# Optimization experiments

Measured on AMD Instinct MI355X. Metric: run time of the kernel, lower is better.

The kernel has to match this reference:

```python
import jax, jax.numpy as jnp
import numpy as np

DIM = 256          # model dim
HK = 8             # kv heads
HQ = 32            # query heads
H = HQ // HK       # queries per kv group
DH = 128           # head dim (== DIM//2, required by RoPE assert)
B = 1
T = 2048
THETA = 10000.0
CACHE = 8192       # RoPE cached seq_len; module uses _freqs_cis[-T:]


def _rope(x):
    # x: [..., T, DH]; positions are the LAST T of the cached 8192 (faithful to _freqs_cis[-T:])
    t = x.shape[-2]
    half = DH  # == DIM // 2
    pos = jnp.arange(CACHE - t, CACHE, dtype=jnp.float32)
    inv_freq = THETA ** (-(jnp.arange(half, dtype=jnp.float32) / half))
    f = pos[:, None] * inv_freq[None, :]            # [T, DH]
    cos, sin = jnp.cos(f), jnp.sin(f)
    x1, x2 = jnp.split(x, 2, axis=-1)
    rot = jnp.concatenate((-x2, x1), axis=-1)       # rotate_half
    return x * cos + rot * sin


def setup_inputs() -> dict:
    key = jax.random.key(0)
    ks = jax.random.split(key, 7)
    q = jax.random.normal(ks[0], (B, T, DIM), jnp.float32)
    k = jax.random.normal(ks[1], (B, T, DIM), jnp.float32)
    v = jax.random.normal(ks[2], (B, T, DIM), jnp.float32)
    mask = jnp.tril(jnp.ones((T, T), dtype=bool))   # causal
    Wq = jax.random.normal(ks[3], (DIM, HQ * DH), jnp.float32) * 0.02
    Wk = jax.random.normal(ks[4], (DIM, HK * DH), jnp.float32) * 0.02
    Wv = jax.random.normal(ks[5], (DIM, HK * DH), jnp.float32) * 0.02
    Wo = jax.random.normal(ks[6], (HQ * DH, DIM), jnp.float32) * 0.02
    return {"q": q, "k": k, "v": v, "mask": mask, "Wq": Wq, "Wk": Wk, "Wv": Wv, "Wo": Wo}


def reference(q, k, v, mask, Wq, Wk, Wv, Wo):
    b, t, _ = q.shape
    # projections + head split; query heads grouped as (HK, H)
    qi = (q @ Wq).reshape(b, t, HQ, DH).transpose(0, 2, 1, 3).reshape(b, HK, H, t, DH)
    ki = (k @ Wk).reshape(b, t, HK, DH).transpose(0, 2, 1, 3)  # [b, HK, t, DH]
    vi = (v @ Wv).reshape(b, t, HK, DH).transpose(0, 2, 1, 3)  # [b, HK, t, DH]
    # RoPE on q, k AND v (module applies _apply_rope to all three)
    qi = _rope(qi)
    ki = _rope(ki)
    vi = _rope(vi)
    s = jnp.einsum('bghid,bgjd->bghij', qi, ki) / jnp.sqrt(jnp.asarray(DH, qi.dtype))
    neg = -jnp.finfo(s.dtype).max
    s = jnp.where(mask, s, neg)
    attn = jax.nn.softmax(s, axis=-1)               # [b, HK, H, t, t]
    vals = jnp.einsum('bghij,bgjd->bghid', attn, vi)
    vals = vals.transpose(0, 3, 1, 2, 4).reshape(b, t, HQ * DH)
    return vals @ Wo
```

## Files before the change

kernel.cpp:

```cpp
#include <hip/hip_runtime.h>
#include <hip/hip_bf16.h>
#include <math.h>

#define TSEQ 2048
#define NHQ 32
#define NHK 8
#define DH 128

typedef __attribute__((ext_vector_type(8))) short short8;
typedef __attribute__((ext_vector_type(4))) float f32x4;
typedef __attribute__((ext_vector_type(4))) short s16x4;

__device__ __forceinline__ short f2bf(float f) {
  union { float f; unsigned u; } v; v.f = f;
  unsigned r = v.u + 0x7fffu + ((v.u >> 16) & 1u);
  return (short)(r >> 16);
}

__device__ __forceinline__ f32x4 zero4() {
  f32x4 z; z[0] = 0.f; z[1] = 0.f; z[2] = 0.f; z[3] = 0.f; return z;
}

__device__ __forceinline__ void async_cp16(const short* g, short* l) {
  __builtin_amdgcn_global_load_lds(
      (const __attribute__((address_space(1))) unsigned int*)g,
      (__attribute__((address_space(3))) unsigned int*)l, 16, 0, 0);
}

__global__ __launch_bounds__(256) void prep_transpose_kernel(
    const float* __restrict__ q, const float* __restrict__ k,
    const float* __restrict__ v, short* __restrict__ qkv,
    float* __restrict__ cosT, float* __restrict__ sinT,
    const float* __restrict__ Wq, const float* __restrict__ Wk,
    const float* __restrict__ Wv, const float* __restrict__ Wo,
    short* __restrict__ WqT, short* __restrict__ WkT,
    short* __restrict__ WvT, short* __restrict__ WoT) {
  __shared__ short tl[64][65];
  int bx = blockIdx.x, tid = threadIdx.x;
  if (bx < 1792) {
    int gid = bx * 256 + tid;
    if (gid < 393216) {
      int i4 = gid * 4;
      const float* src = (i4 < 524288) ? (q + i4)
                       : (i4 < 1048576 ? (k + i4 - 524288) : (v + i4 - 1048576));
      float f0 = src[0], f1 = src[1], f2 = src[2], f3 = src[3];
      s16x4 o; o[0] = f2bf(f0); o[1] = f2bf(f1); o[2] = f2bf(f2); o[3] = f2bf(f3);
      *(s16x4*)&qkv[i4] = o;
    } else if (gid < 458752) {
      int idx = (gid - 393216) * 4;
      int t = idx >> 7, d0 = idx & 127;
      float pos = (float)(8192 - TSEQ + t);
#pragma unroll
      for (int jj = 0; jj < 4; ++jj) {
        int d = d0 + jj;
        float inv = exp2f(-0.10381025296522977f * (float)d);
        float f = pos * inv;
        cosT[t * 128 + d] = cosf(f);
        sinT[t * 128 + d] = sinf(f);
      }
    }
    return;
  }
  int b = bx - 1792;
  const float* S; short* D; int K, N, tr, tc;
  if (b < 256)      { S = Wq; D = WqT; K = 256;  N = 4096; tr = b >> 6;        tc = b & 63; }
  else if (b < 320) { S = Wk; D = WkT; K = 256;  N = 1024; int t = b - 256; tr = t >> 4; tc = t & 15; }
  else if (b < 384) { S = Wv; D = WvT; K = 256;  N = 1024; int t = b - 320; tr = t >> 4; tc = t & 15; }
  else              { S = Wo; D = WoT; K = 4096; N = 256;  int t = b - 384; tr = t >> 2; tc = t & 3; }
  int k0 = tr * 64, n0 = tc * 64;
#pragma unroll
  for (int it = 0; it < 4; ++it) {
    int r = it * 16 + (tid >> 4), c = (tid & 15) * 4;
    const float* s = &S[(size_t)(k0 + r) * N + n0 + c];
    tl[r][c + 0] = f2bf(s[0]); tl[r][c + 1] = f2bf(s[1]);
    tl[r][c + 2] = f2bf(s[2]); tl[r][c + 3] = f2bf(s[3]);
  }
  __syncthreads();
#pragma unroll
  for (int it = 0; it < 4; ++it) {
    int rr = it * 16 + (tid >> 4), cc = (tid & 15) * 4;
    s16x4 o;
    o[0] = tl[cc + 0][rr]; o[1] = tl[cc + 1][rr];
    o[2] = tl[cc + 2][rr]; o[3] = tl[cc + 3][rr];
    *(s16x4*)&D[(size_t)(n0 + rr) * K + k0 + cc] = o;
  }
}

__global__ __launch_bounds__(256) void proj_kernel(
    const short* __restrict__ qkv,
    const short* __restrict__ WqT, const short* __restrict__ WkT,
    const short* __restrict__ WvT,
    const float* __restrict__ cosT, const float* __restrict__ sinT,
    short* __restrict__ Qr, short* __restrict__ Kr, short* __restrict__ Vt) {
  __shared__ short As[64 * 64];
  __shared__ short Bs[128 * 64];
  int tid = threadIdx.x, lane = tid & 63, w = tid >> 6;
  int i = lane & 15, grp = lane >> 4;
  int bh = blockIdx.y, r0 = blockIdx.x * 64;
  const short* X; const short* Wt; short* dst; int vmode = 0;
  if (bh < 32)      { X = qkv;                Wt = WqT + bh * (128 * 256);        dst = Qr + (size_t)bh * TSEQ * DH; }
  else if (bh < 40) { X = qkv + TSEQ * 256;   Wt = WkT + (bh - 32) * (128 * 256); dst = Kr + (size_t)(bh - 32) * TSEQ * DH; }
  else              { X = qkv + 2 * TSEQ * 256; Wt = WvT + (bh - 40) * (128 * 256); dst = Vt + (size_t)(bh - 40) * DH * TSEQ; vmode = 1; }

  f32x4 acc[8];
#pragma unroll
  for (int n = 0; n < 8; ++n) acc[n] = zero4();

  for (int kc = 0; kc < 4; ++kc) {
    __syncthreads();
    {
      int row = tid >> 2, p = tid & 3;
      const short* src = X + (size_t)(r0 + row) * 256 + kc * 64 + p * 16;
      short8 d0 = *(const short8*)(src);
      short8 d1 = *(const short8*)(src + 8);
      int c0 = p * 2;
      *(short8*)&As[row * 64 + ((c0 ^ (row & 7)) * 8)] = d0;
      *(short8*)&As[row * 64 + (((c0 + 1) ^ (row & 7)) * 8)] = d1;
    }
    {
      int row = tid >> 1, p = tid & 1;
      const short* src = Wt + (size_t)row * 256 + kc * 64 + p * 32;
#pragma unroll
      for (int jj = 0; jj < 4; ++jj) {
        short8 dv = *(const short8*)(src + jj * 8);
        int c0 = p * 4 + jj;
        *(short8*)&Bs[row * 64 + ((c0 ^ (row & 7)) * 8)] = dv;
      }
    }
    __syncthreads();
#pragma unroll
    for (int kc2 = 0; kc2 < 2; ++kc2) {
      short8 a = *(const short8*)&As[(w * 16 + i) * 64 + (((kc2 * 4 + grp) ^ (i & 7)) * 8)];
#pragma unroll
      for (int n = 0; n < 8; ++n) {
        short8 bf = *(const short8*)&Bs[(n * 16 + i) * 64 + (((kc2 * 4 + grp) ^ (i & 7)) * 8)];
        acc[n] = __builtin_amdgcn_mfma_f32_16x16x32_bf16(a, bf, acc[n], 0, 0, 0);
      }
    }
  }
#pragma unroll
  for (int r = 0; r < 4; ++r) {
    int t = r0 + w * 16 + grp * 4 + r;
    const float* cr = cosT + (size_t)t * 128;
    const float* sr = sinT + (size_t)t * 128;
#pragma unroll
    for (int n = 0; n < 8; ++n) {
      int d = n * 16 + i;
      float x = acc[n][r];
      float xp = acc[n ^ 4][r];
      float rot = (n < 4) ? -xp : xp;
      float val = x * cr[d] + rot * sr[d];
      short bv = f2bf(val);
      if (vmode) dst[(size_t)d * TSEQ + t] = bv;
      else       dst[(size_t)t * DH + d] = bv;
    }
  }
}

#define SCALE 0.08838834764831845f

__global__ __launch_bounds__(512, 4) void attn_kernel(
    const short* __restrict__ Qr, const short* __restrict__ Kr,
    const short* __restrict__ Vt, short* __restrict__ Oa) {
  __shared__ __attribute__((aligned(16))) short Ks[64 * 128];
  __shared__ __attribute__((aligned(16))) short Vs[128 * 64];
  __shared__ short Ps[8][16 * 72];
  int tid = threadIdx.x, lane = tid & 63, w = tid >> 6;
  int i = lane & 15, grp = lane >> 4;
  int h = blockIdx.y, hk = h >> 2;
  int qt = 15 - blockIdx.x;
  int q0 = qt * 128;
  const short* Qh = Qr + (size_t)h * TSEQ * DH;
  const short* Kh = Kr + (size_t)hk * TSEQ * DH;
  const short* Vh = Vt + (size_t)hk * DH * TSEQ;

  int qrow = q0 + w * 16 + i;
  short8 qf[4];
#pragma unroll
  for (int c = 0; c < 4; ++c)
    qf[c] = *(const short8*)&Qh[(size_t)qrow * DH + c * 32 + grp * 8];

  f32x4 oacc[8];
#pragma unroll
  for (int n = 0; n < 8; ++n) oacc[n] = zero4();
  float mrow[4], lsum[4];
#pragma unroll
  for (int r = 0; r < 4; ++r) { mrow[r] = -3.0e38f; lsum[r] = 0.0f; }

  int ntiles = 2 * qt + 2;
  int wave_max_row = q0 + w * 16 + 15;
  for (int kt = 0; kt < ntiles; ++kt) {
    int kv0 = kt * 64;
    __syncthreads();
    {
#pragma unroll
      for (int hf = 0; hf < 2; ++hf) {
        int ci = hf * 512 + w * 64 + lane;
        int row = ci >> 4, c = ci & 15;
        const short* src = Kh + (size_t)(kv0 + row) * DH + ((c ^ (row & 15)) << 3);
        async_cp16(src, Ks + hf * 4096 + w * 512);
      }
#pragma unroll
      for (int hf = 0; hf < 2; ++hf) {
        int ci = hf * 512 + w * 64 + lane;
        int row = ci >> 3, c = ci & 7;
        const short* src = Vh + (size_t)row * TSEQ + kv0 + ((c ^ (row & 7)) << 3);
        async_cp16(src, Vs + hf * 4096 + w * 512);
      }
    }
    __syncthreads();
    if (kv0 <= wave_max_row) {
      f32x4 sacc[4];
#pragma unroll
      for (int n = 0; n < 4; ++n) sacc[n] = zero4();
      __builtin_amdgcn_s_setprio(1);
#pragma unroll
      for (int c = 0; c < 4; ++c) {
#pragma unroll
        for (int n = 0; n < 4; ++n) {
          short8 kb = *(const short8*)&Ks[(n * 16 + i) * 128 + (((c * 4 + grp) ^ i) * 8)];
          sacc[n] = __builtin_amdgcn_mfma_f32_16x16x32_bf16(qf[c], kb, sacc[n], 0, 0, 0);
        }
      }
      __builtin_amdgcn_s_setprio(0);
      bool diag = (kt >= ntiles - 2);
      float p_[4][4];
#pragma unroll
      for (int n = 0; n < 4; ++n)
#pragma unroll
        for (int r = 0; r < 4; ++r) {
          float s = sacc[n][r] * SCALE;
          if (diag) {
            int qq = q0 + w * 16 + grp * 4 + r;
            int kk = kv0 + n * 16 + i;
            if (kk > qq) s = -3.0e38f;
          }
          p_[n][r] = s;
        }
      float mnew[4];
#pragma unroll
      for (int r = 0; r < 4; ++r)
        mnew[r] = fmaxf(fmaxf(p_[0][r], p_[1][r]), fmaxf(p_[2][r], p_[3][r]));
#pragma unroll
      for (int off = 1; off <= 8; off <<= 1)
#pragma unroll
        for (int r = 0; r < 4; ++r)
          mnew[r] = fmaxf(mnew[r], __shfl_xor(mnew[r], off));
      bool ok = true;
#pragma unroll
      for (int r = 0; r < 4; ++r) ok = ok && (mnew[r] <= mrow[r] + 8.0f);
      if (!__all(ok ? 1 : 0)) {
#pragma unroll
        for (int r = 0; r < 4; ++r) {
          float mn = fmaxf(mrow[r], mnew[r]);
          float sfv = __expf(mrow[r] - mn);
          mrow[r] = mn;
          lsum[r] *= sfv;
#pragma unroll
          for (int n = 0; n < 8; ++n) oacc[n][r] *= sfv;
        }
      }
#pragma unroll
      for (int n = 0; n < 4; ++n)
#pragma unroll
        for (int r = 0; r < 4; ++r) {
          float p = __expf(p_[n][r] - mrow[r]);
          lsum[r] += p;
          Ps[w][(grp * 4 + r) * 72 + n * 16 + i] = f2bf(p);
        }
      __builtin_amdgcn_s_setprio(1);
#pragma unroll
      for (int kc = 0; kc < 2; ++kc) {
        short8 pa = *(const short8*)&Ps[w][i * 72 + kc * 32 + grp * 8];
#pragma unroll
        for (int n = 0; n < 8; ++n) {
          short8 vb = *(const short8*)&Vs[(n * 16 + i) * 64 + (((kc * 4 + grp) ^ (i & 7)) * 8)];
          oacc[n] = __builtin_amdgcn_mfma_f32_16x16x32_bf16(pa, vb, oacc[n], 0, 0, 0);
        }
      }
      __builtin_amdgcn_s_setprio(0);
    }
  }
#pragma unroll
  for (int off = 1; off <= 8; off <<= 1)
#pragma unroll
    for (int r = 0; r < 4; ++r) lsum[r] += __shfl_xor(lsum[r], off);
#pragma unroll
  for (int r = 0; r < 4; ++r) {
    int t = q0 + w * 16 + grp * 4 + r;
    float inv = 1.0f / lsum[r];
#pragma unroll
    for (int n = 0; n < 8; ++n) {
      int d = n * 16 + i;
      Oa[(size_t)t * 4096 + h * 128 + d] = f2bf(oacc[n][r] * inv);
    }
  }
}

__global__ __launch_bounds__(256) void outproj_kernel(
    const short* __restrict__ Oa, const short* __restrict__ WoT,
    float* __restrict__ Opart) {
  __shared__ short As[128 * 64];
  __shared__ short Bs[64 * 64];
  int tid = threadIdx.x, lane = tid & 63, w = tid >> 6;
  int i = lane & 15, grp = lane >> 4;
  int m0 = blockIdx.x * 128, n0 = blockIdx.y * 64, z = blockIdx.z;
  f32x4 acc[2][4];
#pragma unroll
  for (int mf = 0; mf < 2; ++mf)
#pragma unroll
    for (int nf = 0; nf < 4; ++nf) acc[mf][nf] = zero4();
  for (int kc = z * 16; kc < z * 16 + 16; ++kc) {
    __syncthreads();
    {
      int row = tid >> 1, p = tid & 1;
      const short* src = Oa + (size_t)(m0 + row) * 4096 + kc * 64 + p * 32;
#pragma unroll
      for (int jj = 0; jj < 4; ++jj) {
        short8 dv = *(const short8*)(src + jj * 8);
        int c0 = p * 4 + jj;
        *(short8*)&As[row * 64 + ((c0 ^ (row & 7)) * 8)] = dv;
      }
    }
    {
      int row = tid >> 2, p = tid & 3;
      const short* src = WoT + (size_t)(n0 + row) * 4096 + kc * 64 + p * 16;
      short8 d0 = *(const short8*)src;
      short8 d1 = *(const short8*)(src + 8);
      int c0 = p * 2;
      *(short8*)&Bs[row * 64 + ((c0 ^ (row & 7)) * 8)] = d0;
      *(short8*)&Bs[row * 64 + (((c0 + 1) ^ (row & 7)) * 8)] = d1;
    }
    __syncthreads();
#pragma unroll
    for (int kc2 = 0; kc2 < 2; ++kc2) {
#pragma unroll
      for (int mf = 0; mf < 2; ++mf) {
        short8 a = *(const short8*)&As[(w * 32 + mf * 16 + i) * 64 + (((kc2 * 4 + grp) ^ (i & 7)) * 8)];
#pragma unroll
        for (int nf = 0; nf < 4; ++nf) {
          short8 b = *(const short8*)&Bs[(nf * 16 + i) * 64 + (((kc2 * 4 + grp) ^ (i & 7)) * 8)];
          acc[mf][nf] = __builtin_amdgcn_mfma_f32_16x16x32_bf16(a, b, acc[mf][nf], 0, 0, 0);
        }
      }
    }
  }
  float* dst = Opart + (size_t)z * (TSEQ * 256);
#pragma unroll
  for (int mf = 0; mf < 2; ++mf)
#pragma unroll
    for (int r = 0; r < 4; ++r) {
      int t = m0 + w * 32 + mf * 16 + grp * 4 + r;
#pragma unroll
      for (int nf = 0; nf < 4; ++nf)
        dst[(size_t)t * 256 + n0 + nf * 16 + i] = acc[mf][nf][r];
    }
}

__global__ __launch_bounds__(256) void reduce_kernel(
    const float* __restrict__ Opart, float* __restrict__ out) {
  int gid = blockIdx.x * 256 + threadIdx.x;
  int i4 = gid * 4;
  f32x4 s = *(const f32x4*)&Opart[i4];
#pragma unroll
  for (int z = 1; z < 4; ++z) {
    f32x4 p = *(const f32x4*)&Opart[(size_t)z * (TSEQ * 256) + i4];
    s[0] += p[0]; s[1] += p[1]; s[2] += p[2]; s[3] += p[3];
  }
  *(f32x4*)&out[i4] = s;
}

extern "C" void kernel_launch(void* const* d_in, const int* in_sizes, int n_in,
                              void* d_out, int out_size, void* d_ws, size_t ws_size,
                              hipStream_t stream) {
  const float* q  = (const float*)d_in[0];
  const float* k  = (const float*)d_in[1];
  const float* v  = (const float*)d_in[2];
  const float* Wq = (const float*)d_in[4];
  const float* Wk = (const float*)d_in[5];
  const float* Wv = (const float*)d_in[6];
  const float* Wo = (const float*)d_in[7];
  float* out = (float*)d_out;

  char* p = (char*)d_ws;
  auto take = [&](size_t nbytes) {
    char* r = p; p += (nbytes + 255) & ~(size_t)255; return r;
  };
  short* qkv  = (short*)take(3ull * TSEQ * 256 * 2);
  short* WqT  = (short*)take(4096ull * 256 * 2);
  short* WkT  = (short*)take(1024ull * 256 * 2);
  short* WvT  = (short*)take(1024ull * 256 * 2);
  short* WoT  = (short*)take(256ull * 4096 * 2);
  float* cosT = (float*)take((size_t)TSEQ * 128 * 4);
  float* sinT = (float*)take((size_t)TSEQ * 128 * 4);
  short* Qr   = (short*)take((size_t)NHQ * TSEQ * DH * 2);
  short* Kr   = (short*)take((size_t)NHK * TSEQ * DH * 2);
  short* Vt   = (short*)take((size_t)NHK * TSEQ * DH * 2);
  short* Oa   = (short*)take((size_t)TSEQ * 4096 * 2);
  float* Opart = (float*)Qr;

  hipLaunchKernelGGL(prep_transpose_kernel, dim3(2432), dim3(256), 0, stream,
                     q, k, v, qkv, cosT, sinT,
                     Wq, Wk, Wv, Wo, WqT, WkT, WvT, WoT);
  hipLaunchKernelGGL(proj_kernel, dim3(32, 48), dim3(256), 0, stream,
                     qkv, WqT, WkT, WvT, cosT, sinT, Qr, Kr, Vt);
  hipLaunchKernelGGL(attn_kernel, dim3(16, 32), dim3(512), 0, stream,
                     Qr, Kr, Vt, Oa);
  hipLaunchKernelGGL(outproj_kernel, dim3(16, 4, 4), dim3(256), 0, stream,
                     Oa, WoT, Opart);
  hipLaunchKernelGGL(reduce_kernel, dim3(512), dim3(256), 0, stream,
                     Opart, out);
}
```

Measured before the change: 247.2 us.

## Double-buffer K/V tiles, pair causal query tiles per block, fold scale into Q

The attention kernel now double-buffers K/V tiles in shared memory, issuing the async loads for the next tile before computing the current one and waiting with explicit vmcnt waits and raw barriers. Each block processes two query tiles (qt and 15-qt) so causal work is balanced across 256 blocks, grouped by KV head for cache reuse. The softmax scale is folded into the Q projection epilogue, which removes a per-element multiply. Shared memory doubles and occupancy hints drop to 2 blocks per SM. The hand-written vmcnt counts depend on the exact number of outstanding loads.

```diff
diff --git a/kernel.cpp b/kernel.cpp
--- a/kernel.cpp
+++ b/kernel.cpp
@@ -86,6 +86,8 @@
   }
 }
 
+#define SCALE 0.08838834764831845f
+
 __global__ __launch_bounds__(256) void proj_kernel(
     const short* __restrict__ qkv,
     const short* __restrict__ WqT, const short* __restrict__ WkT,
@@ -98,7 +100,8 @@
   int i = lane & 15, grp = lane >> 4;
   int bh = blockIdx.y, r0 = blockIdx.x * 64;
   const short* X; const short* Wt; short* dst; int vmode = 0;
-  if (bh < 32)      { X = qkv;                Wt = WqT + bh * (128 * 256);        dst = Qr + (size_t)bh * TSEQ * DH; }
+  float oscale = 1.0f;
+  if (bh < 32)      { X = qkv;                Wt = WqT + bh * (128 * 256);        dst = Qr + (size_t)bh * TSEQ * DH; oscale = SCALE; }
   else if (bh < 40) { X = qkv + TSEQ * 256;   Wt = WkT + (bh - 32) * (128 * 256); dst = Kr + (size_t)(bh - 32) * TSEQ * DH; }
   else              { X = qkv + 2 * TSEQ * 256; Wt = WvT + (bh - 40) * (128 * 256); dst = Vt + (size_t)(bh - 40) * DH * TSEQ; vmode = 1; }
 
@@ -149,7 +152,7 @@
       float x = acc[n][r];
       float xp = acc[n ^ 4][r];
       float rot = (n < 4) ? -xp : xp;
-      float val = x * cr[d] + rot * sr[d];
+      float val = (x * cr[d] + rot * sr[d]) * oscale;
       short bv = f2bf(val);
       if (vmode) dst[(size_t)d * TSEQ + t] = bv;
       else       dst[(size_t)t * DH + d] = bv;
@@ -157,142 +160,157 @@
   }
 }
 
-#define SCALE 0.08838834764831845f
-
-__global__ __launch_bounds__(512, 4) void attn_kernel(
+__global__ __launch_bounds__(512, 2) void attn_kernel(
     const short* __restrict__ Qr, const short* __restrict__ Kr,
     const short* __restrict__ Vt, short* __restrict__ Oa) {
-  __shared__ __attribute__((aligned(16))) short Ks[64 * 128];
-  __shared__ __attribute__((aligned(16))) short Vs[128 * 64];
+  __shared__ __attribute__((aligned(16))) short Ks[2][64 * 128];
+  __shared__ __attribute__((aligned(16))) short Vs[2][128 * 64];
   __shared__ short Ps[8][16 * 72];
   int tid = threadIdx.x, lane = tid & 63, w = tid >> 6;
   int i = lane & 15, grp = lane >> 4;
-  int h = blockIdx.y, hk = h >> 2;
-  int qt = 15 - blockIdx.x;
-  int q0 = qt * 128;
+  int b = blockIdx.x;
+  int hk = b & 7, hq = (b >> 3) & 3, pr = b >> 5;
+  int h = hk * 4 + hq;
   const short* Qh = Qr + (size_t)h * TSEQ * DH;
   const short* Kh = Kr + (size_t)hk * TSEQ * DH;
   const short* Vh = Vt + (size_t)hk * DH * TSEQ;
 
-  int qrow = q0 + w * 16 + i;
-  short8 qf[4];
-#pragma unroll
-  for (int c = 0; c < 4; ++c)
-    qf[c] = *(const short8*)&Qh[(size_t)qrow * DH + c * 32 + grp * 8];
-
-  f32x4 oacc[8];
-#pragma unroll
-  for (int n = 0; n < 8; ++n) oacc[n] = zero4();
-  float mrow[4], lsum[4];
-#pragma unroll
-  for (int r = 0; r < 4; ++r) { mrow[r] = -3.0e38f; lsum[r] = 0.0f; }
-
-  int ntiles = 2 * qt + 2;
-  int wave_max_row = q0 + w * 16 + 15;
-  for (int kt = 0; kt < ntiles; ++kt) {
-    int kv0 = kt * 64;
-    __syncthreads();
-    {
+  for (int half = 0; half < 2; ++half) {
+    int qt = half ? pr : (15 - pr);
+    int q0 = qt * 128;
+    int qrow = q0 + w * 16 + i;
+    short8 qf[4];
+#pragma unroll
+    for (int c = 0; c < 4; ++c)
+      qf[c] = *(const short8*)&Qh[(size_t)qrow * DH + c * 32 + grp * 8];
+
+    f32x4 oacc[8];
+#pragma unroll
+    for (int n = 0; n < 8; ++n) oacc[n] = zero4();
+    float mrow[4], lsum[4];
+#pragma unroll
+    for (int r = 0; r < 4; ++r) { mrow[r] = -3.0e38f; lsum[r] = 0.0f; }
+
+    int nt = 2 * qt + 2;
+    int wave_max_row = q0 + w * 16 + 15;
+
+    auto stage = [&](int kt_, int bsel) {
+      int kv0_ = kt_ * 64;
 #pragma unroll
       for (int hf = 0; hf < 2; ++hf) {
         int ci = hf * 512 + w * 64 + lane;
         int row = ci >> 4, c = ci & 15;
-        const short* src = Kh + (size_t)(kv0 + row) * DH + ((c ^ (row & 15)) << 3);
-        async_cp16(src, Ks + hf * 4096 + w * 512);
+        async_cp16(Kh + (size_t)(kv0_ + row) * DH + ((c ^ (row & 15)) << 3),
+                   &Ks[bsel][hf * 4096 + w * 512]);
       }
 #pragma unroll
       for (int hf = 0; hf < 2; ++hf) {
         int ci = hf * 512 + w * 64 + lane;
         int row = ci >> 3, c = ci & 7;
-        const short* src = Vh + (size_t)row * TSEQ + kv0 + ((c ^ (row & 7)) << 3);
-        async_cp16(src, Vs + hf * 4096 + w * 512);
-      }
-    }
-    __syncthreads();
-    if (kv0 <= wave_max_row) {
-      f32x4 sacc[4];
-#pragma unroll
-      for (int n = 0; n < 4; ++n) sacc[n] = zero4();
-      __builtin_amdgcn_s_setprio(1);
-#pragma unroll
-      for (int c = 0; c < 4; ++c) {
-#pragma unroll
-        for (int n = 0; n < 4; ++n) {
-          short8 kb = *(const short8*)&Ks[(n * 16 + i) * 128 + (((c * 4 + grp) ^ i) * 8)];
-          sacc[n] = __builtin_amdgcn_mfma_f32_16x16x32_bf16(qf[c], kb, sacc[n], 0, 0, 0);
+        async_cp16(Vh + (size_t)row * TSEQ + kv0_ + ((c ^ (row & 7)) << 3),
+                   &Vs[bsel][hf * 4096 + w * 512]);
+      }
+    };
+
+    stage(0, 0);
+    for (int kt = 0; kt < nt; ++kt) {
+      int kv0 = kt * 64;
+      int buf = kt & 1;
+      if (kt + 1 < nt) {
+        stage(kt + 1, buf ^ 1);
+        asm volatile("s_waitcnt vmcnt(4)" ::: "memory");
+      } else {
+        asm volatile("s_waitcnt vmcnt(0)" ::: "memory");
+      }
+      __builtin_amdgcn_s_barrier();
+      if (kv0 <= wave_max_row) {
+        const short* Kb = &Ks[buf][0];
+        const short* Vb = &Vs[buf][0];
+        f32x4 sacc[4];
+#pragma unroll
+        for (int n = 0; n < 4; ++n) sacc[n] = zero4();
+        __builtin_amdgcn_s_setprio(1);
+#pragma unroll
+        for (int c = 0; c < 4; ++c) {
+#pragma unroll
+          for (int n = 0; n < 4; ++n) {
+            short8 kb = *(const short8*)&Kb[(n * 16 + i) * 128 + (((c * 4 + grp) ^ i) * 8)];
+            sacc[n] = __builtin_amdgcn_mfma_f32_16x16x32_bf16(qf[c], kb, sacc[n], 0, 0, 0);
+          }
         }
-      }
-      __builtin_amdgcn_s_setprio(0);
-      bool diag = (kt >= ntiles - 2);
-      float p_[4][4];
-#pragma unroll
-      for (int n = 0; n < 4; ++n)
-#pragma unroll
-        for (int r = 0; r < 4; ++r) {
-          float s = sacc[n][r] * SCALE;
-          if (diag) {
-            int qq = q0 + w * 16 + grp * 4 + r;
-            int kk = kv0 + n * 16 + i;
-            if (kk > qq) s = -3.0e38f;
+        __builtin_amdgcn_s_setprio(0);
+        bool diag = (kt >= nt - 2);
+        float p_[4][4];
+#pragma unroll
+        for (int n = 0; n < 4; ++n)
+#pragma unroll
+          for (int r = 0; r < 4; ++r) {
+            float s = sacc[n][r];
+            if (diag) {
+              int qq = q0 + w * 16 + grp * 4 + r;
+              int kk = kv0 + n * 16 + i;
+              if (kk > qq) s = -3.0e38f;
+            }
+            p_[n][r] = s;
           }
-          p_[n][r] = s;
+        float mnew[4];
+#pragma unroll
+        for (int r = 0; r < 4; ++r)
+          mnew[r] = fmaxf(fmaxf(p_[0][r], p_[1][r]), fmaxf(p_[2][r], p_[3][r]));
+#pragma unroll
+        for (int off = 1; off <= 8; off <<= 1)
+#pragma unroll
+          for (int r = 0; r < 4; ++r)
+            mnew[r] = fmaxf(mnew[r], __shfl_xor(mnew[r], off));
+        bool ok = true;
+#pragma unroll
+        for (int r = 0; r < 4; ++r) ok = ok && (mnew[r] <= mrow[r] + 8.0f);
+        if (!__all(ok ? 1 : 0)) {
+#pragma unroll
+          for (int r = 0; r < 4; ++r) {
+            float mn = fmaxf(mrow[r], mnew[r]);
+            float sfv = __expf(mrow[r] - mn);
+            mrow[r] = mn;
+            lsum[r] *= sfv;
+#pragma unroll
+            for (int n = 0; n < 8; ++n) oacc[n][r] *= sfv;
+          }
         }
-      float mnew[4];
-#pragma unroll
-      for (int r = 0; r < 4; ++r)
-        mnew[r] = fmaxf(fmaxf(p_[0][r], p_[1][r]), fmaxf(p_[2][r], p_[3][r]));
-#pragma unroll
-      for (int off = 1; off <= 8; off <<= 1)
-#pragma unroll
-        for (int r = 0; r < 4; ++r)
-          mnew[r] = fmaxf(mnew[r], __shfl_xor(mnew[r], off));
-      bool ok = true;
-#pragma unroll
-      for (int r = 0; r < 4; ++r) ok = ok && (mnew[r] <= mrow[r] + 8.0f);
-      if (!__all(ok ? 1 : 0)) {
-#pragma unroll
-        for (int r = 0; r < 4; ++r) {
-          float mn = fmaxf(mrow[r], mnew[r]);
-          float sfv = __expf(mrow[r] - mn);
-          mrow[r] = mn;
-          lsum[r] *= sfv;
-#pragma unroll
-          for (int n = 0; n < 8; ++n) oacc[n][r] *= sfv;
+#pragma unroll
+        for (int n = 0; n < 4; ++n)
+#pragma unroll
+          for (int r = 0; r < 4; ++r) {
+            float p = __expf(p_[n][r] - mrow[r]);
+            lsum[r] += p;
+            Ps[w][(grp * 4 + r) * 72 + n * 16 + i] = f2bf(p);
+          }
+        __builtin_amdgcn_s_setprio(1);
+#pragma unroll
+        for (int kc = 0; kc < 2; ++kc) {
+          short8 pa = *(const short8*)&Ps[w][i * 72 + kc * 32 + grp * 8];
+#pragma unroll
+          for (int n = 0; n < 8; ++n) {
+            short8 vb = *(const short8*)&Vb[(n * 16 + i) * 64 + (((kc * 4 + grp) ^ (i & 7)) * 8)];
+            oacc[n] = __builtin_amdgcn_mfma_f32_16x16x32_bf16(pa, vb, oacc[n], 0, 0, 0);
+          }
         }
-      }
-#pragma unroll
-      for (int n = 0; n < 4; ++n)
-#pragma unroll
-        for (int r = 0; r < 4; ++r) {
-          float p = __expf(p_[n][r] - mrow[r]);
-          lsum[r] += p;
-          Ps[w][(grp * 4 + r) * 72 + n * 16 + i] = f2bf(p);
-        }
-      __builtin_amdgcn_s_setprio(1);
-#pragma unroll
-      for (int kc = 0; kc < 2; ++kc) {
-        short8 pa = *(const short8*)&Ps[w][i * 72 + kc * 32 + grp * 8];
-#pragma unroll
-        for (int n = 0; n < 8; ++n) {
-          short8 vb = *(const short8*)&Vs[(n * 16 + i) * 64 + (((kc * 4 + grp) ^ (i & 7)) * 8)];
-          oacc[n] = __builtin_amdgcn_mfma_f32_16x16x32_bf16(pa, vb, oacc[n], 0, 0, 0);
-        }
-      }
-      __builtin_amdgcn_s_setprio(0);
-    }
-  }
-#pragma unroll
-  for (int off = 1; off <= 8; off <<= 1)
-#pragma unroll
-    for (int r = 0; r < 4; ++r) lsum[r] += __shfl_xor(lsum[r], off);
-#pragma unroll
-  for (int r = 0; r < 4; ++r) {
-    int t = q0 + w * 16 + grp * 4 + r;
-    float inv = 1.0f / lsum[r];
-#pragma unroll
-    for (int n = 0; n < 8; ++n) {
-      int d = n * 16 + i;
-      Oa[(size_t)t * 4096 + h * 128 + d] = f2bf(oacc[n][r] * inv);
+        __builtin_amdgcn_s_setprio(0);
+      }
+      __builtin_amdgcn_s_barrier();
+    }
+#pragma unroll
+    for (int off = 1; off <= 8; off <<= 1)
+#pragma unroll
+      for (int r = 0; r < 4; ++r) lsum[r] += __shfl_xor(lsum[r], off);
+#pragma unroll
+    for (int r = 0; r < 4; ++r) {
+      int t = q0 + w * 16 + grp * 4 + r;
+      float inv = 1.0f / lsum[r];
+#pragma unroll
+      for (int n = 0; n < 8; ++n) {
+        int d = n * 16 + i;
+        Oa[(size_t)t * 4096 + h * 128 + d] = f2bf(oacc[n][r] * inv);
+      }
     }
   }
 }
@@ -404,7 +422,7 @@
                      Wq, Wk, Wv, Wo, WqT, WkT, WvT, WoT);
   hipLaunchKernelGGL(proj_kernel, dim3(32, 48), dim3(256), 0, stream,
                      qkv, WqT, WkT, WvT, cosT, sinT, Qr, Kr, Vt);
-  hipLaunchKernelGGL(attn_kernel, dim3(16, 32), dim3(512), 0, stream,
+  hipLaunchKernelGGL(attn_kernel, dim3(256), dim3(512), 0, stream,
                      Qr, Kr, Vt, Oa);
   hipLaunchKernelGGL(outproj_kernel, dim3(16, 4, 4), dim3(256), 0, stream,
                      Oa, WoT, Opart);
```

Result: faster. 228.2 us (-7.7%).
